# Performance work log

Hardware: AMD Instinct MI355X
Metric: run time of the kernel (lower is better)

The kernel has to match this reference:

```python
import jax, jax.numpy as jnp
import numpy as np

B, S, D = 2, 4096, 1024
H = 16
HD = D // H  # 64


def setup_inputs() -> dict:
    key = jax.random.key(0)
    ks = jax.random.split(key, 5)
    scale = 1.0 / np.sqrt(D)
    return {
        "x": jax.random.normal(ks[0], (B, S, D), dtype=jnp.float32),
        "Wq": jax.random.normal(ks[1], (D, D), dtype=jnp.float32) * scale,
        "Wk": jax.random.normal(ks[2], (D, D), dtype=jnp.float32) * scale,
        "Wv": jax.random.normal(ks[3], (D, D), dtype=jnp.float32) * scale,
        "Wo": jax.random.normal(ks[4], (D, D), dtype=jnp.float32) * scale,
        "bo": jnp.zeros((D,), dtype=jnp.float32),
    }


def reference(x, Wq, Wk, Wv, Wo, bo):
    b, s, d = x.shape
    # Linear layers (torch layout: weight [out, in], y = x @ W.T)
    q = (x @ Wq.T).reshape(b, s, H, HD)
    k = (x @ Wk.T).reshape(b, s, H, HD)
    v = (x @ Wv.T).reshape(b, s, H, HD)
    # scores: [b, h, q, k]
    scores = jnp.einsum("bqhd,bkhd->bhqk", q, k)
    # causal mask (upper triangle above diagonal -> -inf)
    causal = jnp.triu(jnp.ones((s, s), dtype=bool), k=1)
    scores = jnp.where(causal[None, None], -jnp.inf, scores)
    weights = jax.nn.softmax(scores / np.sqrt(HD), axis=-1)  # dropout p=0.0 -> identity
    ctx = jnp.einsum("bhqk,bkhd->bqhd", weights, v).reshape(b, s, d)
    return ctx @ Wo.T + bo
```

## Files before the change

kernel.cpp:

```cpp
#include <hip/hip_runtime.h>
#include <stdint.h>
#include <stddef.h>

#define S_LEN 4096
#define NHEAD 16
#define HDIM 64
#define DMODEL 1024
#define NBATCH 2
#define LOG2E 1.4426950408889634f

typedef __attribute__((ext_vector_type(8))) short bf16x8;
typedef __attribute__((ext_vector_type(4))) float f32x4;
typedef __attribute__((ext_vector_type(16))) float f32x16;
typedef __attribute__((ext_vector_type(2))) unsigned int uint2v;
typedef __attribute__((ext_vector_type(4))) unsigned int uint4v;

__device__ inline unsigned short f2b(float f) {
    union { float f; unsigned int u; } x; x.f = f;
    unsigned int r = (x.u + 0x7fffu + ((x.u >> 16) & 1u)) >> 16;
    return (unsigned short)r;
}

__device__ inline unsigned cvt_pk_bf16(float lo, float hi) {
    unsigned r;
    asm("v_cvt_pk_bf16_f32 %0, %1, %2" : "=v"(r) : "v"(lo), "v"(hi));
    return r;
}

__device__ inline void gload_lds16(const void* g, void* l) {
    __builtin_amdgcn_global_load_lds((const __attribute__((address_space(1))) void*)g,
                                     (__attribute__((address_space(3))) void*)l,
                                     16, 0, 0);
}

__global__ void cvt_x(const float* __restrict__ in, unsigned short* __restrict__ out, int n4) {
    int i = blockIdx.x * 256 + threadIdx.x;
    if (i >= n4) return;
    float4 v = ((const float4*)in)[i];
    ushort4 o;
    o.x = f2b(v.x); o.y = f2b(v.y); o.z = f2b(v.z); o.w = f2b(v.w);
    ((ushort4*)out)[i] = o;
}

__global__ void cvt_w(const float* __restrict__ w0, const float* __restrict__ w1,
                      const float* __restrict__ w2, const float* __restrict__ w3,
                      unsigned short* __restrict__ dst) {
    int z = blockIdx.y;
    const float* src = (z == 0) ? w0 : (z == 1) ? w1 : (z == 2) ? w2 : w3;
    int i = blockIdx.x * 256 + threadIdx.x;
    float4 v = ((const float4*)src)[i];
    ushort4 o;
    o.x = f2b(v.x); o.y = f2b(v.y); o.z = f2b(v.z); o.w = f2b(v.w);
    ((ushort4*)(dst + (size_t)z * DMODEL * DMODEL))[i] = o;
}

__global__ __launch_bounds__(256, 2)
void gemm_qkv(const unsigned short* __restrict__ xb,
              const unsigned short* __restrict__ wqb,
              const unsigned short* __restrict__ wkb,
              const unsigned short* __restrict__ wvb,
              unsigned short* __restrict__ Qb,
              unsigned short* __restrict__ Kb,
              unsigned short* __restrict__ Vt,
              float qscale) {
    __shared__ unsigned short Asl[128 * 64];
    __shared__ unsigned short Bsl[128 * 64];
    const int tid  = threadIdx.x;
    const int lane = tid & 63;
    const int wid  = tid >> 6;
    const int wm   = (wid >> 1) * 64, wn = (wid & 1) * 64;
    const int lr   = lane & 15, lk = lane >> 4;
    const int z    = blockIdx.z;

    const unsigned short* A;
    const unsigned short* Bw;
    int m0, n0;
    if (z < 2) { A = xb; Bw = z ? wkb : wqb; m0 = blockIdx.x * 128; n0 = blockIdx.y * 128; }
    else       { A = wvb; Bw = xb;           m0 = blockIdx.y * 128; n0 = blockIdx.x * 128; }

    f32x4 acc[4][4];
#pragma unroll
    for (int i = 0; i < 4; ++i)
#pragma unroll
        for (int j = 0; j < 4; ++j) acc[i][j] = (f32x4){0.f, 0.f, 0.f, 0.f};

    for (int kt = 0; kt < DMODEL; kt += 64) {
#pragma unroll
        for (int i = 0; i < 4; ++i) {
            int c = i * 256 + tid;
            int r = c >> 3, gc = (c & 7) ^ (r & 7);
            gload_lds16(A + (size_t)(m0 + r) * DMODEL + kt + gc * 8, Asl + c * 8);
        }
#pragma unroll
        for (int i = 0; i < 4; ++i) {
            int c = i * 256 + tid;
            int r = c >> 3, gc = (c & 7) ^ (r & 7);
            gload_lds16(Bw + (size_t)(n0 + r) * DMODEL + kt + gc * 8, Bsl + c * 8);
        }
        __syncthreads();
#pragma unroll
        for (int kh = 0; kh < 2; ++kh) {
            int cl = kh * 4 + lk;
            bf16x8 af[4], bfr[4];
#pragma unroll
            for (int m = 0; m < 4; ++m) {
                int r = wm + m * 16 + lr;
                af[m] = *(const bf16x8*)(Asl + r * 64 + ((cl ^ (r & 7)) * 8));
            }
#pragma unroll
            for (int n = 0; n < 4; ++n) {
                int r = wn + n * 16 + lr;
                bfr[n] = *(const bf16x8*)(Bsl + r * 64 + ((cl ^ (r & 7)) * 8));
            }
#pragma unroll
            for (int m = 0; m < 4; ++m)
#pragma unroll
                for (int n = 0; n < 4; ++n)
                    acc[m][n] = __builtin_amdgcn_mfma_f32_16x16x32_bf16(af[m], bfr[n], acc[m][n], 0, 0, 0);
        }
        __syncthreads();
    }

#pragma unroll
    for (int m = 0; m < 4; ++m) {
#pragma unroll
        for (int n = 0; n < 4; ++n) {
            int gn = n0 + wn + n * 16 + lr;
#pragma unroll
            for (int r = 0; r < 4; ++r) {
                int gm = m0 + wm + m * 16 + lk * 4 + r;
                float v = acc[m][n][r];
                if (z == 0) {
                    int b = gm >> 12, s = gm & 4095, h = gn >> 6, hd = gn & 63;
                    Qb[((size_t)((b * NHEAD + h) * S_LEN + s)) * HDIM + hd] = f2b(v * qscale);
                } else if (z == 1) {
                    int b = gm >> 12, s = gm & 4095, h = gn >> 6, hd = gn & 63;
                    Kb[((size_t)((b * NHEAD + h) * S_LEN + s)) * HDIM + hd] = f2b(v);
                } else {
                    int h = gm >> 6, hd = gm & 63, b = gn >> 12, s = gn & 4095;
                    Vt[((size_t)((b * NHEAD + h) * HDIM + hd)) * S_LEN + s] = f2b(v);
                }
            }
        }
    }
}

__global__ __launch_bounds__(256, 2)
void gemm_out(const unsigned short* __restrict__ A,
              const unsigned short* __restrict__ Bw,
              float* __restrict__ out, const float* __restrict__ bias) {
    __shared__ unsigned short Asl[128 * 64];
    __shared__ unsigned short Bsl[128 * 64];
    const int tid  = threadIdx.x;
    const int lane = tid & 63;
    const int wid  = tid >> 6;
    const int wm   = (wid >> 1) * 64, wn = (wid & 1) * 64;
    const int lr   = lane & 15, lk = lane >> 4;
    const int m0   = blockIdx.x * 128, n0 = blockIdx.y * 128;

    f32x4 acc[4][4];
#pragma unroll
    for (int i = 0; i < 4; ++i)
#pragma unroll
        for (int j = 0; j < 4; ++j) acc[i][j] = (f32x4){0.f, 0.f, 0.f, 0.f};

    for (int kt = 0; kt < DMODEL; kt += 64) {
#pragma unroll
        for (int i = 0; i < 4; ++i) {
            int c = i * 256 + tid;
            int r = c >> 3, gc = (c & 7) ^ (r & 7);
            gload_lds16(A + (size_t)(m0 + r) * DMODEL + kt + gc * 8, Asl + c * 8);
        }
#pragma unroll
        for (int i = 0; i < 4; ++i) {
            int c = i * 256 + tid;
            int r = c >> 3, gc = (c & 7) ^ (r & 7);
            gload_lds16(Bw + (size_t)(n0 + r) * DMODEL + kt + gc * 8, Bsl + c * 8);
        }
        __syncthreads();
#pragma unroll
        for (int kh = 0; kh < 2; ++kh) {
            int cl = kh * 4 + lk;
            bf16x8 af[4], bfr[4];
#pragma unroll
            for (int m = 0; m < 4; ++m) {
                int r = wm + m * 16 + lr;
                af[m] = *(const bf16x8*)(Asl + r * 64 + ((cl ^ (r & 7)) * 8));
            }
#pragma unroll
            for (int n = 0; n < 4; ++n) {
                int r = wn + n * 16 + lr;
                bfr[n] = *(const bf16x8*)(Bsl + r * 64 + ((cl ^ (r & 7)) * 8));
            }
#pragma unroll
            for (int m = 0; m < 4; ++m)
#pragma unroll
                for (int n = 0; n < 4; ++n)
                    acc[m][n] = __builtin_amdgcn_mfma_f32_16x16x32_bf16(af[m], bfr[n], acc[m][n], 0, 0, 0);
        }
        __syncthreads();
    }
#pragma unroll
    for (int m = 0; m < 4; ++m)
#pragma unroll
        for (int n = 0; n < 4; ++n) {
            int gn = n0 + wn + n * 16 + lr;
#pragma unroll
            for (int r = 0; r < 4; ++r) {
                int gm = m0 + wm + m * 16 + lk * 4 + r;
                out[(size_t)gm * DMODEL + gn] = acc[m][n][r] + bias[gn];
            }
        }
}

__global__ __launch_bounds__(256)
void attn_fwd(const unsigned short* __restrict__ Q,
              const unsigned short* __restrict__ K,
              const unsigned short* __restrict__ Vt,
              unsigned short* __restrict__ ctx) {
    __shared__ unsigned short Kl[2][4096];
    __shared__ unsigned short Vl[2][4096];

    const int tid  = threadIdx.x;
    const int lane = tid & 63;
    const int w    = tid >> 6;
    const int l31  = lane & 31;
    const int hi   = lane >> 5;

    const int bid  = blockIdx.x;
    const int qt   = 31 - (bid >> 5);
    const int bh   = bid & 31;
    const int b    = bh >> 4, h = bh & 15;
    const int q0   = qt * 128;
    const int qw0  = q0 + w * 32;

    const unsigned short* Qh = Q  + (size_t)bh * S_LEN * HDIM;
    const unsigned short* Kh = K  + (size_t)bh * S_LEN * HDIM;
    const unsigned short* Vh = Vt + (size_t)bh * HDIM * S_LEN;

    const int skA  = tid >> 6;
    const int lS   = tid & 63;
    const int lS31 = lS & 31, hiS = lS >> 5;
    const unsigned short* kb0 = Kh + (size_t)lS31 * HDIM + skA * 16 + hiS * 8;
    const unsigned short* kb1 = Kh + (size_t)(32 + lS31) * HDIM + skA * 16 + hiS * 8;
    const unsigned short* vb0 = Vh + (size_t)lS31 * S_LEN + skA * 16 + hiS * 8;
    const unsigned short* vb1 = Vh + (size_t)(32 + lS31) * S_LEN + skA * 16 + hiS * 8;

    bf16x8 qf[4];
    {
        const unsigned short* qrow = Qh + (size_t)(qw0 + l31) * HDIM + hi * 8;
#pragma unroll
        for (int s = 0; s < 4; ++s) qf[s] = *(const bf16x8*)(qrow + s * 16);
    }

    bf16x8 ones;
#pragma unroll
    for (int j = 0; j < 8; ++j) ones[j] = (short)0x3F80;

    const unsigned short* KL = &Kl[0][0] + lane * 8;
    const unsigned short* VL = &Vl[0][0] + lane * 8;

    f32x16 o0, o1, ls;
#pragma unroll
    for (int j = 0; j < 16; ++j) { o0[j] = 0.f; o1[j] = 0.f; ls[j] = 0.f; }

    const int nt = 2 * qt + 2;

    auto stage = [&](int buf, int kv0) {
        gload_lds16(kb0 + (size_t)kv0 * HDIM, &Kl[buf][(size_t)tid * 8]);
        gload_lds16(kb1 + (size_t)kv0 * HDIM, &Kl[buf][2048 + (size_t)tid * 8]);
        gload_lds16(vb0 + kv0, &Vl[buf][(size_t)tid * 8]);
        gload_lds16(vb1 + kv0, &Vl[buf][2048 + (size_t)tid * 8]);
    };

    auto packfrag = [&](float v0, float v1, float v2, float v3,
                        float v4, float v5, float v6, float v7) -> bf16x8 {
        unsigned a0 = cvt_pk_bf16(v0, v1), a1 = cvt_pk_bf16(v2, v3);
        unsigned b0 = cvt_pk_bf16(v4, v5), b1 = cvt_pk_bf16(v6, v7);
        uint2v r0 = __builtin_amdgcn_permlane32_swap(a0, b0, false, false);
        uint2v r1 = __builtin_amdgcn_permlane32_swap(a1, b1, false, false);
        uint4v f; f.x = r0.x; f.y = r1.x; f.z = r0.y; f.w = r1.y;
        return __builtin_bit_cast(bf16x8, f);
    };

    auto compute = [&](int buf, int kv0) {
        const unsigned short* KB = KL + buf * 4096;
        const unsigned short* VB = VL + buf * 4096;
        const int q = qw0 + l31;

        if (kv0 < qw0 + 32) {
            f32x16 st;
#pragma unroll
            for (int j = 0; j < 16; ++j) st[j] = 0.f;
            __builtin_amdgcn_s_setprio(1);
#pragma unroll
            for (int s = 0; s < 4; ++s)
                st = __builtin_amdgcn_mfma_f32_32x32x16_bf16(
                        *(const bf16x8*)(KB + s * 512), qf[s], st, 0, 0, 0);
            __builtin_amdgcn_s_setprio(0);
            if (kv0 + 31 > qw0) {
#pragma unroll
                for (int j = 0; j < 16; ++j) {
                    int roff = (j & 3) + 8 * (j >> 2) + 4 * hi;
                    if (kv0 + roff > q) st[j] = -3e38f;
                }
            }
#pragma unroll
            for (int j = 0; j < 16; ++j) st[j] = exp2f(st[j]);
            bf16x8 pa = packfrag(st[0], st[1], st[2], st[3], st[4], st[5], st[6], st[7]);
            bf16x8 pb = packfrag(st[8], st[9], st[10], st[11], st[12], st[13], st[14], st[15]);
            __builtin_amdgcn_s_setprio(1);
            ls = __builtin_amdgcn_mfma_f32_32x32x16_bf16(ones, pa, ls, 0, 0, 0);
            ls = __builtin_amdgcn_mfma_f32_32x32x16_bf16(ones, pb, ls, 0, 0, 0);
            o0 = __builtin_amdgcn_mfma_f32_32x32x16_bf16(*(const bf16x8*)(VB + 0 * 512), pa, o0, 0, 0, 0);
            o1 = __builtin_amdgcn_mfma_f32_32x32x16_bf16(*(const bf16x8*)(VB + 4 * 512), pa, o1, 0, 0, 0);
            o0 = __builtin_amdgcn_mfma_f32_32x32x16_bf16(*(const bf16x8*)(VB + 1 * 512), pb, o0, 0, 0, 0);
            o1 = __builtin_amdgcn_mfma_f32_32x32x16_bf16(*(const bf16x8*)(VB + 5 * 512), pb, o1, 0, 0, 0);
            __builtin_amdgcn_s_setprio(0);
        }

        if (kv0 < qw0) {
            f32x16 st;
#pragma unroll
            for (int j = 0; j < 16; ++j) st[j] = 0.f;
            __builtin_amdgcn_s_setprio(1);
#pragma unroll
            for (int s = 0; s < 4; ++s)
                st = __builtin_amdgcn_mfma_f32_32x32x16_bf16(
                        *(const bf16x8*)(KB + (4 + s) * 512), qf[s], st, 0, 0, 0);
            __builtin_amdgcn_s_setprio(0);
            if (kv0 + 63 > qw0) {
#pragma unroll
                for (int j = 0; j < 16; ++j) {
                    int roff = (j & 3) + 8 * (j >> 2) + 4 * hi;
                    if (kv0 + 32 + roff > q) st[j] = -3e38f;
                }
            }
#pragma unroll
            for (int j = 0; j < 16; ++j) st[j] = exp2f(st[j]);
            bf16x8 pa = packfrag(st[0], st[1], st[2], st[3], st[4], st[5], st[6], st[7]);
            bf16x8 pb = packfrag(st[8], st[9], st[10], st[11], st[12], st[13], st[14], st[15]);
            __builtin_amdgcn_s_setprio(1);
            ls = __builtin_amdgcn_mfma_f32_32x32x16_bf16(ones, pa, ls, 0, 0, 0);
            ls = __builtin_amdgcn_mfma_f32_32x32x16_bf16(ones, pb, ls, 0, 0, 0);
            o0 = __builtin_amdgcn_mfma_f32_32x32x16_bf16(*(const bf16x8*)(VB + 2 * 512), pa, o0, 0, 0, 0);
            o1 = __builtin_amdgcn_mfma_f32_32x32x16_bf16(*(const bf16x8*)(VB + 6 * 512), pa, o1, 0, 0, 0);
            o0 = __builtin_amdgcn_mfma_f32_32x32x16_bf16(*(const bf16x8*)(VB + 3 * 512), pb, o0, 0, 0, 0);
            o1 = __builtin_amdgcn_mfma_f32_32x32x16_bf16(*(const bf16x8*)(VB + 7 * 512), pb, o1, 0, 0, 0);
            __builtin_amdgcn_s_setprio(0);
        }
    };

    stage(0, 0);
    __syncthreads();
    for (int t = 0; t < nt; t += 2) {
        const int kv0 = t * 64;
        stage(1, kv0 + 64);
        compute(0, kv0);
        __syncthreads();
        if (t + 2 < nt) stage(0, kv0 + 128);
        compute(1, kv0 + 64);
        __syncthreads();
    }

    float inv = 1.f / ls[0];
    size_t sq = (size_t)q0 + w * 32 + l31;
    unsigned short* crow = ctx + ((size_t)b * S_LEN + sq) * DMODEL + h * HDIM;
#pragma unroll
    for (int quad = 0; quad < 4; ++quad) {
        int hdbase = quad * 8 + hi * 4;
        unsigned w0 = cvt_pk_bf16(o0[4 * quad] * inv, o0[4 * quad + 1] * inv);
        unsigned w1 = cvt_pk_bf16(o0[4 * quad + 2] * inv, o0[4 * quad + 3] * inv);
        *(unsigned long long*)(crow + hdbase) = ((unsigned long long)w1 << 32) | w0;
        unsigned w2 = cvt_pk_bf16(o1[4 * quad] * inv, o1[4 * quad + 1] * inv);
        unsigned w3 = cvt_pk_bf16(o1[4 * quad + 2] * inv, o1[4 * quad + 3] * inv);
        *(unsigned long long*)(crow + 32 + hdbase) = ((unsigned long long)w3 << 32) | w2;
    }
}

extern "C" void kernel_launch(void* const* d_in, const int* in_sizes, int n_in,
                              void* d_out, int out_size, void* d_ws, size_t ws_size,
                              hipStream_t stream) {
    (void)in_sizes; (void)n_in; (void)out_size; (void)ws_size;
    const float* x  = (const float*)d_in[0];
    const float* Wq = (const float*)d_in[1];
    const float* Wk = (const float*)d_in[2];
    const float* Wv = (const float*)d_in[3];
    const float* Wo = (const float*)d_in[4];
    const float* bo = (const float*)d_in[5];

    unsigned short* ws  = (unsigned short*)d_ws;
    const size_t NTOK = (size_t)NBATCH * S_LEN;
    unsigned short* xb  = ws;
    unsigned short* wqb = xb  + NTOK * DMODEL;
    unsigned short* wkb = wqb + (size_t)DMODEL * DMODEL;
    unsigned short* wvb = wkb + (size_t)DMODEL * DMODEL;
    unsigned short* wob = wvb + (size_t)DMODEL * DMODEL;
    unsigned short* Qb  = wob + (size_t)DMODEL * DMODEL;
    unsigned short* Kb  = Qb  + NTOK * DMODEL;
    unsigned short* Vt  = Kb  + NTOK * DMODEL;
    unsigned short* ctx = xb;

    int n4x = (int)(NTOK * DMODEL / 4);
    cvt_x<<<(n4x + 255) / 256, 256, 0, stream>>>(x, xb, n4x);
    cvt_w<<<dim3(DMODEL * DMODEL / 4 / 256, 4), 256, 0, stream>>>(Wq, Wk, Wv, Wo, wqb);

    const float qscale = 0.125f * LOG2E;
    gemm_qkv<<<dim3(64, 8, 3), 256, 0, stream>>>(xb, wqb, wkb, wvb, Qb, Kb, Vt, qscale);

    attn_fwd<<<1024, 256, 0, stream>>>(Qb, Kb, Vt, ctx);

    gemm_out<<<dim3(64, 8), 256, 0, stream>>>(ctx, wob, (float*)d_out, bo);
}
```

Before: 211.2 us.

## Replace MFMA row-sum with VALU tree sum and add unmasked fast path

The softmax denominator was computed with two extra MFMAs per 32-key block against a vector of ones. It is now summed on the vector ALU per lane with a tree reduction plus one final permlane32 swap. A compute_full path handles KV tiles lying entirely below the diagonal: it issues both QK^T MFMA chains together and skips the mask checks, leaving the masked version for diagonal tiles only. This frees matrix-unit cycles at the cost of extra VALU adds, and the sum is now taken from fp32 probabilities rather than the bf16-rounded ones used in the PV product.

New measurement: 224.9 us. 6.5% more time.

```diff
diff --git a/kernel.cpp b/kernel.cpp
--- a/kernel.cpp
+++ b/kernel.cpp
@@ -25,6 +25,11 @@
     unsigned r;
     asm("v_cvt_pk_bf16_f32 %0, %1, %2" : "=v"(r) : "v"(lo), "v"(hi));
     return r;
+}
+
+__device__ inline float xadd32(float v) {
+    uint2v r = __builtin_amdgcn_permlane32_swap(__float_as_uint(v), __float_as_uint(v), false, false);
+    return __uint_as_float(r.x) + __uint_as_float(r.y);
 }
 
 __device__ inline void gload_lds16(const void* g, void* l) {
@@ -253,16 +258,13 @@
         for (int s = 0; s < 4; ++s) qf[s] = *(const bf16x8*)(qrow + s * 16);
     }
 
-    bf16x8 ones;
-#pragma unroll
-    for (int j = 0; j < 8; ++j) ones[j] = (short)0x3F80;
-
     const unsigned short* KL = &Kl[0][0] + lane * 8;
     const unsigned short* VL = &Vl[0][0] + lane * 8;
 
-    f32x16 o0, o1, ls;
-#pragma unroll
-    for (int j = 0; j < 16; ++j) { o0[j] = 0.f; o1[j] = 0.f; ls[j] = 0.f; }
+    f32x16 o0, o1;
+#pragma unroll
+    for (int j = 0; j < 16; ++j) { o0[j] = 0.f; o1[j] = 0.f; }
+    float ps = 0.f;
 
     const int nt = 2 * qt + 2;
 
@@ -273,17 +275,61 @@
         gload_lds16(vb1 + kv0, &Vl[buf][2048 + (size_t)tid * 8]);
     };
 
-    auto packfrag = [&](float v0, float v1, float v2, float v3,
-                        float v4, float v5, float v6, float v7) -> bf16x8 {
-        unsigned a0 = cvt_pk_bf16(v0, v1), a1 = cvt_pk_bf16(v2, v3);
-        unsigned b0 = cvt_pk_bf16(v4, v5), b1 = cvt_pk_bf16(v6, v7);
+    auto packfrag = [&](const f32x16& v, int base) -> bf16x8 {
+        unsigned a0 = cvt_pk_bf16(v[base + 0], v[base + 1]), a1 = cvt_pk_bf16(v[base + 2], v[base + 3]);
+        unsigned b0 = cvt_pk_bf16(v[base + 4], v[base + 5]), b1 = cvt_pk_bf16(v[base + 6], v[base + 7]);
         uint2v r0 = __builtin_amdgcn_permlane32_swap(a0, b0, false, false);
         uint2v r1 = __builtin_amdgcn_permlane32_swap(a1, b1, false, false);
         uint4v f; f.x = r0.x; f.y = r1.x; f.z = r0.y; f.w = r1.y;
         return __builtin_bit_cast(bf16x8, f);
     };
 
-    auto compute = [&](int buf, int kv0) {
+    auto treesum = [&](const f32x16& v) -> float {
+        float s01 = (v[0] + v[1]) + (v[2] + v[3]);
+        float s23 = (v[4] + v[5]) + (v[6] + v[7]);
+        float s45 = (v[8] + v[9]) + (v[10] + v[11]);
+        float s67 = (v[12] + v[13]) + (v[14] + v[15]);
+        return (s01 + s23) + (s45 + s67);
+    };
+
+    auto compute_full = [&](int buf, int kv0) {
+        const unsigned short* KB = KL + buf * 4096;
+        const unsigned short* VB = VL + buf * 4096;
+        f32x16 sa, sb;
+#pragma unroll
+        for (int j = 0; j < 16; ++j) { sa[j] = 0.f; sb[j] = 0.f; }
+        __builtin_amdgcn_s_setprio(1);
+#pragma unroll
+        for (int s = 0; s < 4; ++s) {
+            sa = __builtin_amdgcn_mfma_f32_32x32x16_bf16(*(const bf16x8*)(KB + s * 512), qf[s], sa, 0, 0, 0);
+            sb = __builtin_amdgcn_mfma_f32_32x32x16_bf16(*(const bf16x8*)(KB + (4 + s) * 512), qf[s], sb, 0, 0, 0);
+        }
+        __builtin_amdgcn_s_setprio(0);
+#pragma unroll
+        for (int j = 0; j < 16; ++j) sa[j] = exp2f(sa[j]);
+        ps += treesum(sa);
+        bf16x8 pa = packfrag(sa, 0);
+        bf16x8 pb = packfrag(sa, 8);
+        __builtin_amdgcn_s_setprio(1);
+        o0 = __builtin_amdgcn_mfma_f32_32x32x16_bf16(*(const bf16x8*)(VB + 0 * 512), pa, o0, 0, 0, 0);
+        o1 = __builtin_amdgcn_mfma_f32_32x32x16_bf16(*(const bf16x8*)(VB + 4 * 512), pa, o1, 0, 0, 0);
+        o0 = __builtin_amdgcn_mfma_f32_32x32x16_bf16(*(const bf16x8*)(VB + 1 * 512), pb, o0, 0, 0, 0);
+        o1 = __builtin_amdgcn_mfma_f32_32x32x16_bf16(*(const bf16x8*)(VB + 5 * 512), pb, o1, 0, 0, 0);
+        __builtin_amdgcn_s_setprio(0);
+#pragma unroll
+        for (int j = 0; j < 16; ++j) sb[j] = exp2f(sb[j]);
+        ps += treesum(sb);
+        bf16x8 pc = packfrag(sb, 0);
+        bf16x8 pd = packfrag(sb, 8);
+        __builtin_amdgcn_s_setprio(1);
+        o0 = __builtin_amdgcn_mfma_f32_32x32x16_bf16(*(const bf16x8*)(VB + 2 * 512), pc, o0, 0, 0, 0);
+        o1 = __builtin_amdgcn_mfma_f32_32x32x16_bf16(*(const bf16x8*)(VB + 6 * 512), pc, o1, 0, 0, 0);
+        o0 = __builtin_amdgcn_mfma_f32_32x32x16_bf16(*(const bf16x8*)(VB + 3 * 512), pd, o0, 0, 0, 0);
+        o1 = __builtin_amdgcn_mfma_f32_32x32x16_bf16(*(const bf16x8*)(VB + 7 * 512), pd, o1, 0, 0, 0);
+        __builtin_amdgcn_s_setprio(0);
+    };
+
+    auto compute_edge = [&](int buf, int kv0) {
         const unsigned short* KB = KL + buf * 4096;
         const unsigned short* VB = VL + buf * 4096;
         const int q = qw0 + l31;
@@ -295,8 +341,7 @@
             __builtin_amdgcn_s_setprio(1);
 #pragma unroll
             for (int s = 0; s < 4; ++s)
-                st = __builtin_amdgcn_mfma_f32_32x32x16_bf16(
-                        *(const bf16x8*)(KB + s * 512), qf[s], st, 0, 0, 0);
+                st = __builtin_amdgcn_mfma_f32_32x32x16_bf16(*(const bf16x8*)(KB + s * 512), qf[s], st, 0, 0, 0);
             __builtin_amdgcn_s_setprio(0);
             if (kv0 + 31 > qw0) {
 #pragma unroll
@@ -307,11 +352,10 @@
             }
 #pragma unroll
             for (int j = 0; j < 16; ++j) st[j] = exp2f(st[j]);
-            bf16x8 pa = packfrag(st[0], st[1], st[2], st[3], st[4], st[5], st[6], st[7]);
-            bf16x8 pb = packfrag(st[8], st[9], st[10], st[11], st[12], st[13], st[14], st[15]);
+            ps += treesum(st);
+            bf16x8 pa = packfrag(st, 0);
+            bf16x8 pb = packfrag(st, 8);
             __builtin_amdgcn_s_setprio(1);
-            ls = __builtin_amdgcn_mfma_f32_32x32x16_bf16(ones, pa, ls, 0, 0, 0);
-            ls = __builtin_amdgcn_mfma_f32_32x32x16_bf16(ones, pb, ls, 0, 0, 0);
             o0 = __builtin_amdgcn_mfma_f32_32x32x16_bf16(*(const bf16x8*)(VB + 0 * 512), pa, o0, 0, 0, 0);
             o1 = __builtin_amdgcn_mfma_f32_32x32x16_bf16(*(const bf16x8*)(VB + 4 * 512), pa, o1, 0, 0, 0);
             o0 = __builtin_amdgcn_mfma_f32_32x32x16_bf16(*(const bf16x8*)(VB + 1 * 512), pb, o0, 0, 0, 0);
@@ -326,8 +370,7 @@
             __builtin_amdgcn_s_setprio(1);
 #pragma unroll
             for (int s = 0; s < 4; ++s)
-                st = __builtin_amdgcn_mfma_f32_32x32x16_bf16(
-                        *(const bf16x8*)(KB + (4 + s) * 512), qf[s], st, 0, 0, 0);
+                st = __builtin_amdgcn_mfma_f32_32x32x16_bf16(*(const bf16x8*)(KB + (4 + s) * 512), qf[s], st, 0, 0, 0);
             __builtin_amdgcn_s_setprio(0);
             if (kv0 + 63 > qw0) {
 #pragma unroll
@@ -338,11 +381,10 @@
             }
 #pragma unroll
             for (int j = 0; j < 16; ++j) st[j] = exp2f(st[j]);
-            bf16x8 pa = packfrag(st[0], st[1], st[2], st[3], st[4], st[5], st[6], st[7]);
-            bf16x8 pb = packfrag(st[8], st[9], st[10], st[11], st[12], st[13], st[14], st[15]);
+            ps += treesum(st);
+            bf16x8 pa = packfrag(st, 0);
+            bf16x8 pb = packfrag(st, 8);
             __builtin_amdgcn_s_setprio(1);
-            ls = __builtin_amdgcn_mfma_f32_32x32x16_bf16(ones, pa, ls, 0, 0, 0);
-            ls = __builtin_amdgcn_mfma_f32_32x32x16_bf16(ones, pb, ls, 0, 0, 0);
             o0 = __builtin_amdgcn_mfma_f32_32x32x16_bf16(*(const bf16x8*)(VB + 2 * 512), pa, o0, 0, 0, 0);
             o1 = __builtin_amdgcn_mfma_f32_32x32x16_bf16(*(const bf16x8*)(VB + 6 * 512), pa, o1, 0, 0, 0);
             o0 = __builtin_amdgcn_mfma_f32_32x32x16_bf16(*(const bf16x8*)(VB + 3 * 512), pb, o0, 0, 0, 0);
@@ -356,14 +398,15 @@
     for (int t = 0; t < nt; t += 2) {
         const int kv0 = t * 64;
         stage(1, kv0 + 64);
-        compute(0, kv0);
+        if (kv0 + 63 <= qw0) compute_full(0, kv0); else compute_edge(0, kv0);
         __syncthreads();
         if (t + 2 < nt) stage(0, kv0 + 128);
-        compute(1, kv0 + 64);
-        __syncthreads();
-    }
-
-    float inv = 1.f / ls[0];
+        if (kv0 + 127 <= qw0) compute_full(1, kv0 + 64); else compute_edge(1, kv0 + 64);
+        __syncthreads();
+    }
+
+    float lsum = xadd32(ps);
+    float inv = 1.f / lsum;
     size_t sq = (size_t)q0 + w * 32 + l31;
     unsigned short* crow = ctx + ((size_t)b * S_LEN + sq) * DMODEL + h * HDIM;
 #pragma unroll
```

## Use raw v_exp_f32, seed QK MFMA from zero vector, remap head order

Applied to the files above, without the earlier changes.

Replaces exp2f with inline v_exp_f32, which drops the range and denormal handling that exp2f adds. The first QK MFMA now takes a shared zero accumulator instead of re-zeroing a register vector on every tile. Block-to-(batch,head) mapping is permuted so that neighbouring blocks work on different heads, which changes L2 locality across the GPU's dies. The raw exp instruction may flush denormal results, which is harmless here because the masked scores are -3e38.

New measurement: 193.5 us. 1.09x faster.

```diff
diff --git a/kernel.cpp b/kernel.cpp
--- a/kernel.cpp
+++ b/kernel.cpp
@@ -24,6 +24,12 @@
 __device__ inline unsigned cvt_pk_bf16(float lo, float hi) {
     unsigned r;
     asm("v_cvt_pk_bf16_f32 %0, %1, %2" : "=v"(r) : "v"(lo), "v"(hi));
+    return r;
+}
+
+__device__ inline float exp_fast(float x) {
+    float r;
+    asm("v_exp_f32 %0, %1" : "=v"(r) : "v"(x));
     return r;
 }
 
@@ -229,7 +235,7 @@
 
     const int bid  = blockIdx.x;
     const int qt   = 31 - (bid >> 5);
-    const int bh   = bid & 31;
+    const int bh   = ((bid & 7) << 2) | ((bid >> 3) & 3);
     const int b    = bh >> 4, h = bh & 15;
     const int q0   = qt * 128;
     const int qw0  = q0 + w * 32;
@@ -257,6 +263,10 @@
 #pragma unroll
     for (int j = 0; j < 8; ++j) ones[j] = (short)0x3F80;
 
+    f32x16 z16;
+#pragma unroll
+    for (int j = 0; j < 16; ++j) z16[j] = 0.f;
+
     const unsigned short* KL = &Kl[0][0] + lane * 8;
     const unsigned short* VL = &Vl[0][0] + lane * 8;
 
@@ -273,10 +283,9 @@
         gload_lds16(vb1 + kv0, &Vl[buf][2048 + (size_t)tid * 8]);
     };
 
-    auto packfrag = [&](float v0, float v1, float v2, float v3,
-                        float v4, float v5, float v6, float v7) -> bf16x8 {
-        unsigned a0 = cvt_pk_bf16(v0, v1), a1 = cvt_pk_bf16(v2, v3);
-        unsigned b0 = cvt_pk_bf16(v4, v5), b1 = cvt_pk_bf16(v6, v7);
+    auto packfrag = [&](const f32x16& v, int base) -> bf16x8 {
+        unsigned a0 = cvt_pk_bf16(v[base + 0], v[base + 1]), a1 = cvt_pk_bf16(v[base + 2], v[base + 3]);
+        unsigned b0 = cvt_pk_bf16(v[base + 4], v[base + 5]), b1 = cvt_pk_bf16(v[base + 6], v[base + 7]);
         uint2v r0 = __builtin_amdgcn_permlane32_swap(a0, b0, false, false);
         uint2v r1 = __builtin_amdgcn_permlane32_swap(a1, b1, false, false);
         uint4v f; f.x = r0.x; f.y = r1.x; f.z = r0.y; f.w = r1.y;
@@ -289,12 +298,11 @@
         const int q = qw0 + l31;
 
         if (kv0 < qw0 + 32) {
-            f32x16 st;
-#pragma unroll
-            for (int j = 0; j < 16; ++j) st[j] = 0.f;
             __builtin_amdgcn_s_setprio(1);
-#pragma unroll
-            for (int s = 0; s < 4; ++s)
+            f32x16 st = __builtin_amdgcn_mfma_f32_32x32x16_bf16(
+                            *(const bf16x8*)(KB + 0 * 512), qf[0], z16, 0, 0, 0);
+#pragma unroll
+            for (int s = 1; s < 4; ++s)
                 st = __builtin_amdgcn_mfma_f32_32x32x16_bf16(
                         *(const bf16x8*)(KB + s * 512), qf[s], st, 0, 0, 0);
             __builtin_amdgcn_s_setprio(0);
@@ -306,9 +314,9 @@
                 }
             }
 #pragma unroll
-            for (int j = 0; j < 16; ++j) st[j] = exp2f(st[j]);
-            bf16x8 pa = packfrag(st[0], st[1], st[2], st[3], st[4], st[5], st[6], st[7]);
-            bf16x8 pb = packfrag(st[8], st[9], st[10], st[11], st[12], st[13], st[14], st[15]);
+            for (int j = 0; j < 16; ++j) st[j] = exp_fast(st[j]);
+            bf16x8 pa = packfrag(st, 0);
+            bf16x8 pb = packfrag(st, 8);
             __builtin_amdgcn_s_setprio(1);
             ls = __builtin_amdgcn_mfma_f32_32x32x16_bf16(ones, pa, ls, 0, 0, 0);
             ls = __builtin_amdgcn_mfma_f32_32x32x16_bf16(ones, pb, ls, 0, 0, 0);
@@ -320,12 +328,11 @@
         }
 
         if (kv0 < qw0) {
-            f32x16 st;
-#pragma unroll
-            for (int j = 0; j < 16; ++j) st[j] = 0.f;
             __builtin_amdgcn_s_setprio(1);
-#pragma unroll
-            for (int s = 0; s < 4; ++s)
+            f32x16 st = __builtin_amdgcn_mfma_f32_32x32x16_bf16(
+                            *(const bf16x8*)(KB + 4 * 512), qf[0], z16, 0, 0, 0);
+#pragma unroll
+            for (int s = 1; s < 4; ++s)
                 st = __builtin_amdgcn_mfma_f32_32x32x16_bf16(
                         *(const bf16x8*)(KB + (4 + s) * 512), qf[s], st, 0, 0, 0);
             __builtin_amdgcn_s_setprio(0);
@@ -337,9 +344,9 @@
                 }
             }
 #pragma unroll
-            for (int j = 0; j < 16; ++j) st[j] = exp2f(st[j]);
-            bf16x8 pa = packfrag(st[0], st[1], st[2], st[3], st[4], st[5], st[6], st[7]);
-            bf16x8 pb = packfrag(st[8], st[9], st[10], st[11], st[12], st[13], st[14], st[15]);
+            for (int j = 0; j < 16; ++j) st[j] = exp_fast(st[j]);
+            bf16x8 pa = packfrag(st, 0);
+            bf16x8 pb = packfrag(st, 8);
             __builtin_amdgcn_s_setprio(1);
             ls = __builtin_amdgcn_mfma_f32_32x32x16_bf16(ones, pa, ls, 0, 0, 0);
             ls = __builtin_amdgcn_mfma_f32_32x32x16_bf16(ones, pb, ls, 0, 0, 0);
```
